# Kernel optimization log

Measured on AMD Instinct MI355X. Metric: run time of the kernel, lower is better.

## Reference

```python
import jax, jax.numpy as jnp
import numpy as np

NEG_SLOPE = 0.2  # LeakyReLU slope used by default activation_attn


def setup_inputs() -> dict:
    key = jax.random.key(0)
    k1, k2, k3, k4, k5 = jax.random.split(key, 5)
    N, K, F, H, D = 50000, 16, 128, 8, 64
    s = 1.0 / np.sqrt(F)  # roughly torch Linear init scale
    return {
        "x_self": jax.random.normal(k1, (N, F), dtype=jnp.float32),
        "x_neigh": jax.random.normal(k2, (N, K, F), dtype=jnp.float32),
        "W": jax.random.normal(k3, (H, F, D), dtype=jnp.float32) * s,
        "a_self": jax.random.normal(k4, (H, F), dtype=jnp.float32) * s,
        "a_neigh": jax.random.normal(k5, (H, F), dtype=jnp.float32) * s,
    }


def reference(x_self, x_neigh, W, a_self, a_neigh):
    # x_self: [N, F], x_neigh: [N, K, F]
    # x_all = concat(self, neigh) along neighbor axis -> [N, K+1, F]
    x_all = jnp.concatenate([x_self[:, None, :], x_neigh], axis=1)
    # per-head attention logits (each head's fc_attn_* is Linear(F, 1), no bias)
    logit_self = jnp.einsum('nf,hf->nh', x_self, a_self)          # [N, H]
    logit_all = jnp.einsum('nkf,hf->nkh', x_all, a_neigh)         # [N, K+1, H]
    logits = logit_self[:, None, :] + logit_all                   # [N, K+1, H]
    logits = jnp.where(logits >= 0, logits, NEG_SLOPE * logits)   # LeakyReLU(0.2)
    attn = jax.nn.softmax(logits, axis=1)                         # softmax over neighbors
    # per-head projection of all nodes: Linear(F, D), no bias
    xw = jnp.einsum('nkf,hfd->nkhd', x_all, W)                    # [N, K+1, H, D]
    h = jnp.einsum('nkhd,nkh->nhd', xw, attn)                     # [N, H, D]
    N, H, D = h.shape
    # concat aggregation: heads stacked along feature dim (head 0 first)
    return h.reshape(N, H * D)
```

## Files before the change

kernel.cpp:

```cpp
#include <hip/hip_runtime.h>

#define NTHREADS 256
#define NB 4
#define K 16
#define KP1 17
#define F 128
#define H 8
#define D 64
#define FP 132
#define NEG_SLOPE 0.2f


__global__ __launch_bounds__(NTHREADS, 4) void gat_kernel(
    const float* __restrict__ x_self,
    const float* __restrict__ x_neigh,
    const float* __restrict__ W,
    const float* __restrict__ a_self,
    const float* __restrict__ a_neigh,
    float* __restrict__ out,
    int N)
{
    __shared__ __align__(16) float xall[NB][KP1][FP];
    __shared__ __align__(16) float attn[NB][KP1][H];
    __shared__ float self_s[NB][H];

    float* yb = (float*)xall;

    const int tid = threadIdx.x;
    const int node0 = blockIdx.x * NB;

    {
        const int tot_self = NB * (F / 4);
        for (int i = tid; i < tot_self; i += NTHREADS) {
            int nb = i / (F / 4);
            int f4 = i % (F / 4);
            if (node0 + nb < N) {
                float4 v = ((const float4*)(x_self + (size_t)(node0 + nb) * F))[f4];
                *(float4*)&xall[nb][0][f4 * 4] = v;
            }
        }
        const int tot_n = NB * K * (F / 4);
        for (int i = tid; i < tot_n; i += NTHREADS) {
            int nb  = i / (K * F / 4);
            int rem = i % (K * F / 4);
            int k   = rem / (F / 4);
            int f4  = rem % (F / 4);
            if (node0 + nb < N) {
                float4 v = ((const float4*)(x_neigh + ((size_t)(node0 + nb) * K + k) * F))[f4];
                *(float4*)&xall[nb][k + 1][f4 * 4] = v;
            }
        }
    }
    __syncthreads();

    {
        const int p  = tid & 7;
        const int h  = (tid >> 3) & 7;
        const int nb = tid >> 6;
        const float* av  = a_neigh + h * F;
        const float* xr0 = &xall[nb][2 * p][0];
        const float* xr1 = &xall[nb][2 * p + 1][0];
        float4 s0 = {0.f, 0.f, 0.f, 0.f}, s1 = s0;
        #pragma unroll 8
        for (int f4 = 0; f4 < F / 4; f4++) {
            float4 avv = ((const float4*)av)[f4];
            float4 x0 = *(const float4*)(xr0 + f4 * 4);
            float4 x1 = *(const float4*)(xr1 + f4 * 4);
            s0.x += x0.x * avv.x; s0.y += x0.y * avv.y;
            s0.z += x0.z * avv.z; s0.w += x0.w * avv.w;
            s1.x += x1.x * avv.x; s1.y += x1.y * avv.y;
            s1.z += x1.z * avv.z; s1.w += x1.w * avv.w;
        }
        attn[nb][2 * p][h]     = (s0.x + s0.y) + (s0.z + s0.w);
        attn[nb][2 * p + 1][h] = (s1.x + s1.y) + (s1.z + s1.w);

        if (tid < 32) {
            const int h2  = tid & 7;
            const int nb2 = tid >> 3;
            const float* avn = a_neigh + h2 * F;
            const float* avs = a_self  + h2 * F;
            const float* x16 = &xall[nb2][16][0];
            const float* xs  = &xall[nb2][0][0];
            float4 t0 = {0.f, 0.f, 0.f, 0.f}, t1 = t0;
            #pragma unroll 8
            for (int f4 = 0; f4 < F / 4; f4++) {
                float4 an = ((const float4*)avn)[f4];
                float4 as = ((const float4*)avs)[f4];
                float4 v0 = *(const float4*)(x16 + f4 * 4);
                float4 v1 = *(const float4*)(xs  + f4 * 4);
                t0.x += v0.x * an.x; t0.y += v0.y * an.y;
                t0.z += v0.z * an.z; t0.w += v0.w * an.w;
                t1.x += v1.x * as.x; t1.y += v1.y * as.y;
                t1.z += v1.z * as.z; t1.w += v1.w * as.w;
            }
            attn[nb2][16][h2] = (t0.x + t0.y) + (t0.z + t0.w);
            self_s[nb2][h2]   = (t1.x + t1.y) + (t1.z + t1.w);
        }
    }
    __syncthreads();

    for (int i = tid; i < NB * H; i += NTHREADS) {
        int nb = i >> 3, h = i & 7;
        float sl = self_s[nb][h];
        float m = -1e30f;
        #pragma unroll
        for (int k = 0; k < KP1; k++) {
            float lg = sl + attn[nb][k][h];
            lg = (lg >= 0.f) ? lg : NEG_SLOPE * lg;
            attn[nb][k][h] = lg;
            m = fmaxf(m, lg);
        }
        float s = 0.f;
        #pragma unroll
        for (int k = 0; k < KP1; k++) {
            float e = __expf(attn[nb][k][h] - m);
            attn[nb][k][h] = e;
            s += e;
        }
        float inv = 1.0f / s;
        #pragma unroll
        for (int k = 0; k < KP1; k++) attn[nb][k][h] *= inv;
    }
    __syncthreads();

    {
        const int h  = (tid >> 5) & 7;
        const int f4 = tid & 31;
        float4 acc[NB];
        #pragma unroll
        for (int j = 0; j < NB; j++) acc[j] = {0.f, 0.f, 0.f, 0.f};
        for (int k = 0; k < KP1; k++) {
            #pragma unroll
            for (int j = 0; j < NB; j++) {
                float a = attn[j][k][h];
                float4 xv = *(const float4*)&xall[j][k][f4 * 4];
                acc[j].x += a * xv.x; acc[j].y += a * xv.y;
                acc[j].z += a * xv.z; acc[j].w += a * xv.w;
            }
        }
        __syncthreads();
        #pragma unroll
        for (int j = 0; j < NB; j++) {
            *(float4*)&yb[((size_t)j * H + h) * F + f4 * 4] = acc[j];
        }
    }
    __syncthreads();

    {
        const int d  = tid & (D - 1);
        const int hg = tid >> 6;
        const float* Wp0 = W + ((size_t)hg * F) * D + d;
        const float* Wp1 = W + ((size_t)(hg + 4) * F) * D + d;
        const float* y00 = &yb[(size_t)(0 * H + hg) * F];
        const float* y01 = &yb[(size_t)(1 * H + hg) * F];
        const float* y02 = &yb[(size_t)(2 * H + hg) * F];
        const float* y03 = &yb[(size_t)(3 * H + hg) * F];
        const float* y10 = &yb[(size_t)(0 * H + hg + 4) * F];
        const float* y11 = &yb[(size_t)(1 * H + hg + 4) * F];
        const float* y12 = &yb[(size_t)(2 * H + hg + 4) * F];
        const float* y13 = &yb[(size_t)(3 * H + hg + 4) * F];

        float a00 = 0.f, a01 = 0.f, a02 = 0.f, a03 = 0.f;
        float a10 = 0.f, a11 = 0.f, a12 = 0.f, a13 = 0.f;

        float cw00 = Wp0[0 * D], cw01 = Wp0[1 * D], cw02 = Wp0[2 * D], cw03 = Wp0[3 * D];
        float cw10 = Wp1[0 * D], cw11 = Wp1[1 * D], cw12 = Wp1[2 * D], cw13 = Wp1[3 * D];

        #pragma unroll 4
        for (int f4 = 0; f4 < F / 4; f4++) {
            const int g = (f4 + 1) & 31;
            float nw00 = Wp0[(g * 4 + 0) * D], nw01 = Wp0[(g * 4 + 1) * D];
            float nw02 = Wp0[(g * 4 + 2) * D], nw03 = Wp0[(g * 4 + 3) * D];
            float nw10 = Wp1[(g * 4 + 0) * D], nw11 = Wp1[(g * 4 + 1) * D];
            float nw12 = Wp1[(g * 4 + 2) * D], nw13 = Wp1[(g * 4 + 3) * D];

            float4 v00 = *(const float4*)(y00 + f4 * 4);
            float4 v01 = *(const float4*)(y01 + f4 * 4);
            float4 v02 = *(const float4*)(y02 + f4 * 4);
            float4 v03 = *(const float4*)(y03 + f4 * 4);
            float4 v10 = *(const float4*)(y10 + f4 * 4);
            float4 v11 = *(const float4*)(y11 + f4 * 4);
            float4 v12 = *(const float4*)(y12 + f4 * 4);
            float4 v13 = *(const float4*)(y13 + f4 * 4);

            a00 += v00.x * cw00 + v00.y * cw01 + v00.z * cw02 + v00.w * cw03;
            a01 += v01.x * cw00 + v01.y * cw01 + v01.z * cw02 + v01.w * cw03;
            a02 += v02.x * cw00 + v02.y * cw01 + v02.z * cw02 + v02.w * cw03;
            a03 += v03.x * cw00 + v03.y * cw01 + v03.z * cw02 + v03.w * cw03;
            a10 += v10.x * cw10 + v10.y * cw11 + v10.z * cw12 + v10.w * cw13;
            a11 += v11.x * cw10 + v11.y * cw11 + v11.z * cw12 + v11.w * cw13;
            a12 += v12.x * cw10 + v12.y * cw11 + v12.z * cw12 + v12.w * cw13;
            a13 += v13.x * cw10 + v13.y * cw11 + v13.z * cw12 + v13.w * cw13;

            cw00 = nw00; cw01 = nw01; cw02 = nw02; cw03 = nw03;
            cw10 = nw10; cw11 = nw11; cw12 = nw12; cw13 = nw13;
        }

        if (node0 + 0 < N) {
            out[(size_t)(node0 + 0) * (H * D) + hg * D + d] = a00;
            out[(size_t)(node0 + 0) * (H * D) + (hg + 4) * D + d] = a10;
        }
        if (node0 + 1 < N) {
            out[(size_t)(node0 + 1) * (H * D) + hg * D + d] = a01;
            out[(size_t)(node0 + 1) * (H * D) + (hg + 4) * D + d] = a11;
        }
        if (node0 + 2 < N) {
            out[(size_t)(node0 + 2) * (H * D) + hg * D + d] = a02;
            out[(size_t)(node0 + 2) * (H * D) + (hg + 4) * D + d] = a12;
        }
        if (node0 + 3 < N) {
            out[(size_t)(node0 + 3) * (H * D) + hg * D + d] = a03;
            out[(size_t)(node0 + 3) * (H * D) + (hg + 4) * D + d] = a13;
        }
    }
}

extern "C" void kernel_launch(void* const* d_in, const int* in_sizes, int n_in,
                              void* d_out, int out_size, void* d_ws, size_t ws_size,
                              hipStream_t stream) {
    const float* x_self  = (const float*)d_in[0];
    const float* x_neigh = (const float*)d_in[1];
    const float* W       = (const float*)d_in[2];
    const float* a_self  = (const float*)d_in[3];
    const float* a_neigh = (const float*)d_in[4];
    float* out = (float*)d_out;

    const int N = in_sizes[0] / F;
    const int nblocks = (N + NB - 1) / NB;
    gat_kernel<<<nblocks, NTHREADS, 0, stream>>>(x_self, x_neigh, W, a_self, a_neigh, out, N);
}
```

Baseline: 842.2 us.

## Split F reduction across lane groups with float4 W loads and shuffle reduce

```diff
diff --git a/kernel.cpp b/kernel.cpp
--- a/kernel.cpp
+++ b/kernel.cpp
@@ -147,70 +147,66 @@
     __syncthreads();
 
     {
-        const int d  = tid & (D - 1);
-        const int hg = tid >> 6;
-        const float* Wp0 = W + ((size_t)hg * F) * D + d;
-        const float* Wp1 = W + ((size_t)(hg + 4) * F) * D + d;
-        const float* y00 = &yb[(size_t)(0 * H + hg) * F];
-        const float* y01 = &yb[(size_t)(1 * H + hg) * F];
-        const float* y02 = &yb[(size_t)(2 * H + hg) * F];
-        const float* y03 = &yb[(size_t)(3 * H + hg) * F];
-        const float* y10 = &yb[(size_t)(0 * H + hg + 4) * F];
-        const float* y11 = &yb[(size_t)(1 * H + hg + 4) * F];
-        const float* y12 = &yb[(size_t)(2 * H + hg + 4) * F];
-        const float* y13 = &yb[(size_t)(3 * H + hg + 4) * F];
-
-        float a00 = 0.f, a01 = 0.f, a02 = 0.f, a03 = 0.f;
-        float a10 = 0.f, a11 = 0.f, a12 = 0.f, a13 = 0.f;
-
-        float cw00 = Wp0[0 * D], cw01 = Wp0[1 * D], cw02 = Wp0[2 * D], cw03 = Wp0[3 * D];
-        float cw10 = Wp1[0 * D], cw11 = Wp1[1 * D], cw12 = Wp1[2 * D], cw13 = Wp1[3 * D];
-
-        #pragma unroll 4
-        for (int f4 = 0; f4 < F / 4; f4++) {
-            const int g = (f4 + 1) & 31;
-            float nw00 = Wp0[(g * 4 + 0) * D], nw01 = Wp0[(g * 4 + 1) * D];
-            float nw02 = Wp0[(g * 4 + 2) * D], nw03 = Wp0[(g * 4 + 3) * D];
-            float nw10 = Wp1[(g * 4 + 0) * D], nw11 = Wp1[(g * 4 + 1) * D];
-            float nw12 = Wp1[(g * 4 + 2) * D], nw13 = Wp1[(g * 4 + 3) * D];
-
-            float4 v00 = *(const float4*)(y00 + f4 * 4);
-            float4 v01 = *(const float4*)(y01 + f4 * 4);
-            float4 v02 = *(const float4*)(y02 + f4 * 4);
-            float4 v03 = *(const float4*)(y03 + f4 * 4);
-            float4 v10 = *(const float4*)(y10 + f4 * 4);
-            float4 v11 = *(const float4*)(y11 + f4 * 4);
-            float4 v12 = *(const float4*)(y12 + f4 * 4);
-            float4 v13 = *(const float4*)(y13 + f4 * 4);
-
-            a00 += v00.x * cw00 + v00.y * cw01 + v00.z * cw02 + v00.w * cw03;
-            a01 += v01.x * cw00 + v01.y * cw01 + v01.z * cw02 + v01.w * cw03;
-            a02 += v02.x * cw00 + v02.y * cw01 + v02.z * cw02 + v02.w * cw03;
-            a03 += v03.x * cw00 + v03.y * cw01 + v03.z * cw02 + v03.w * cw03;
-            a10 += v10.x * cw10 + v10.y * cw11 + v10.z * cw12 + v10.w * cw13;
-            a11 += v11.x * cw10 + v11.y * cw11 + v11.z * cw12 + v11.w * cw13;
-            a12 += v12.x * cw10 + v12.y * cw11 + v12.z * cw12 + v12.w * cw13;
-            a13 += v13.x * cw10 + v13.y * cw11 + v13.z * cw12 + v13.w * cw13;
-
-            cw00 = nw00; cw01 = nw01; cw02 = nw02; cw03 = nw03;
-            cw10 = nw10; cw11 = nw11; cw12 = nw12; cw13 = nw13;
-        }
-
-        if (node0 + 0 < N) {
-            out[(size_t)(node0 + 0) * (H * D) + hg * D + d] = a00;
-            out[(size_t)(node0 + 0) * (H * D) + (hg + 4) * D + d] = a10;
-        }
-        if (node0 + 1 < N) {
-            out[(size_t)(node0 + 1) * (H * D) + hg * D + d] = a01;
-            out[(size_t)(node0 + 1) * (H * D) + (hg + 4) * D + d] = a11;
-        }
-        if (node0 + 2 < N) {
-            out[(size_t)(node0 + 2) * (H * D) + hg * D + d] = a02;
-            out[(size_t)(node0 + 2) * (H * D) + (hg + 4) * D + d] = a12;
-        }
-        if (node0 + 3 < N) {
-            out[(size_t)(node0 + 3) * (H * D) + hg * D + d] = a03;
-            out[(size_t)(node0 + 3) * (H * D) + (hg + 4) * D + d] = a13;
+        const int lane = tid & 63;
+        const int w    = tid >> 6;
+        const int fg   = lane >> 4;
+        const int d4   = lane & 15;
+        const int h0 = w, h1 = w + 4;
+        const float* Wb0 = W + ((size_t)h0 * F) * D + d4 * 4;
+        const float* Wb1 = W + ((size_t)h1 * F) * D + d4 * 4;
+
+        float4 acc0[NB], acc1[NB];
+        #pragma unroll
+        for (int nb = 0; nb < NB; nb++) {
+            acc0[nb] = {0.f, 0.f, 0.f, 0.f};
+            acc1[nb] = {0.f, 0.f, 0.f, 0.f};
+        }
+
+        for (int fb = 0; fb < 8; fb++) {
+            const int f0 = fb * 16 + fg * 4;
+            float4 w0[4], w1[4];
+            #pragma unroll
+            for (int ff = 0; ff < 4; ff++) {
+                w0[ff] = *(const float4*)(Wb0 + (size_t)(f0 + ff) * D);
+                w1[ff] = *(const float4*)(Wb1 + (size_t)(f0 + ff) * D);
+            }
+            float4 y0[NB], y1[NB];
+            #pragma unroll
+            for (int nb = 0; nb < NB; nb++) {
+                y0[nb] = *(const float4*)&yb[((size_t)nb * H + h0) * F + f0];
+                y1[nb] = *(const float4*)&yb[((size_t)nb * H + h1) * F + f0];
+            }
+            #pragma unroll
+            for (int nb = 0; nb < NB; nb++) {
+                acc0[nb].x += y0[nb].x * w0[0].x + y0[nb].y * w0[1].x + y0[nb].z * w0[2].x + y0[nb].w * w0[3].x;
+                acc0[nb].y += y0[nb].x * w0[0].y + y0[nb].y * w0[1].y + y0[nb].z * w0[2].y + y0[nb].w * w0[3].y;
+                acc0[nb].z += y0[nb].x * w0[0].z + y0[nb].y * w0[1].z + y0[nb].z * w0[2].z + y0[nb].w * w0[3].z;
+                acc0[nb].w += y0[nb].x * w0[0].w + y0[nb].y * w0[1].w + y0[nb].z * w0[2].w + y0[nb].w * w0[3].w;
+                acc1[nb].x += y1[nb].x * w1[0].x + y1[nb].y * w1[1].x + y1[nb].z * w1[2].x + y1[nb].w * w1[3].x;
+                acc1[nb].y += y1[nb].x * w1[0].y + y1[nb].y * w1[1].y + y1[nb].z * w1[2].y + y1[nb].w * w1[3].y;
+                acc1[nb].z += y1[nb].x * w1[0].z + y1[nb].y * w1[1].z + y1[nb].z * w1[2].z + y1[nb].w * w1[3].z;
+                acc1[nb].w += y1[nb].x * w1[0].w + y1[nb].y * w1[1].w + y1[nb].z * w1[2].w + y1[nb].w * w1[3].w;
+            }
+        }
+
+        #pragma unroll
+        for (int nb = 0; nb < NB; nb++) {
+            acc0[nb].x += __shfl_xor(acc0[nb].x, 16); acc0[nb].x += __shfl_xor(acc0[nb].x, 32);
+            acc0[nb].y += __shfl_xor(acc0[nb].y, 16); acc0[nb].y += __shfl_xor(acc0[nb].y, 32);
+            acc0[nb].z += __shfl_xor(acc0[nb].z, 16); acc0[nb].z += __shfl_xor(acc0[nb].z, 32);
+            acc0[nb].w += __shfl_xor(acc0[nb].w, 16); acc0[nb].w += __shfl_xor(acc0[nb].w, 32);
+            acc1[nb].x += __shfl_xor(acc1[nb].x, 16); acc1[nb].x += __shfl_xor(acc1[nb].x, 32);
+            acc1[nb].y += __shfl_xor(acc1[nb].y, 16); acc1[nb].y += __shfl_xor(acc1[nb].y, 32);
+            acc1[nb].z += __shfl_xor(acc1[nb].z, 16); acc1[nb].z += __shfl_xor(acc1[nb].z, 32);
+            acc1[nb].w += __shfl_xor(acc1[nb].w, 16); acc1[nb].w += __shfl_xor(acc1[nb].w, 32);
+        }
+
+        #pragma unroll
+        for (int nb = 0; nb < NB; nb++) {
+            if (fg == nb && node0 + nb < N) {
+                *(float4*)&out[(size_t)(node0 + nb) * (H * D) + h0 * D + d4 * 4] = acc0[nb];
+                *(float4*)&out[(size_t)(node0 + nb) * (H * D) + h1 * D + d4 * 4] = acc1[nb];
+            }
         }
     }
 }
```

New measurement: 782.6 us. 7.1% less time.
